# Kernel tuning notes

Measured on AMD Instinct MI355X. Metric: run time of the kernel, lower is better.

## Reference

```python
import jax, jax.numpy as jnp
import numpy as np

WS = 4        # window_size
HEADS = 12    # num_heads


def setup_inputs() -> dict:
    key = jax.random.key(0)
    k1, k2, k3 = jax.random.split(key, 3)
    B, N, E = 32, 4096, 384
    x = jax.random.normal(k1, (B, N, E), dtype=jnp.float32)
    w_in = jax.random.normal(k2, (3 * E, E), dtype=jnp.float32) * 0.02
    b_in = jnp.zeros((3 * E,), dtype=jnp.float32)
    w_out = jax.random.normal(k3, (E, E), dtype=jnp.float32) * 0.02
    b_out = jnp.zeros((E,), dtype=jnp.float32)
    return {"x": x, "w_in": w_in, "b_in": b_in, "w_out": w_out, "b_out": b_out}


def reference(x, w_in, b_in, w_out, b_out):
    B, N, E = x.shape
    H = W = int(np.sqrt(N))
    nh, nw = H // WS, W // WS
    hd = E // HEADS
    T = WS * WS  # tokens per window

    # window partition: [B, H, W, E] -> [B*nh*nw, T, E]
    xw = x.reshape(B, nh, WS, nw, WS, E)
    xw = xw.transpose(0, 1, 3, 2, 4, 5).reshape(-1, T, E)

    # packed QKV projection (torch nn.MultiheadAttention in_proj)
    qkv = xw @ w_in.T + b_in                      # [nWin, T, 3E]
    q, k, v = jnp.split(qkv, 3, axis=-1)          # each [nWin, T, E]

    def split_heads(t):
        return t.reshape(-1, T, HEADS, hd).transpose(0, 2, 1, 3)  # [nWin, h, T, hd]

    q, k, v = split_heads(q), split_heads(k), split_heads(v)
    scale = 1.0 / np.sqrt(hd).astype(np.float32)
    scores = jnp.einsum('whqd,whkd->whqk', q * scale, k)          # [nWin, h, T, T]
    attn = jax.nn.softmax(scores, axis=-1)
    out = jnp.einsum('whqk,whkd->whqd', attn, v)                  # [nWin, h, T, hd]
    out = out.transpose(0, 2, 1, 3).reshape(-1, T, E)
    out = out @ w_out.T + b_out                                   # out_proj

    # window reverse: [B*nh*nw, T, E] -> [B, N, E]
    out = out.reshape(B, nh, nw, WS, WS, E)
    out = out.transpose(0, 1, 3, 2, 4, 5).reshape(B, N, E)
    return out
```

## Files before the change

### kernel.cpp

```cpp
#include <hip/hip_runtime.h>
#include <hip/hip_bf16.h>

typedef __attribute__((ext_vector_type(8))) short short8;
typedef __attribute__((ext_vector_type(4))) float f32x4;

static __device__ __forceinline__ f32x4 MFMA16(short8 a, short8 b, f32x4 c) {
    return __builtin_amdgcn_mfma_f32_16x16x32_bf16(a, b, c, 0, 0, 0);
}
static __device__ __forceinline__ unsigned short f2bf(float f) {
    union { __hip_bfloat16 h; unsigned short u; } c;
    c.h = __float2bfloat16(f);
    return c.u;
}
static __device__ __forceinline__ void gload16(const void* g, void* l) {
    __builtin_amdgcn_global_load_lds(
        (const __attribute__((address_space(1))) unsigned int*)g,
        (__attribute__((address_space(3))) unsigned int*)l, 16, 0, 0);
}

constexpr size_t kWstOff = 0;
constexpr size_t kWosOff = 884736;
constexpr size_t kBrrOff = 1179648;
constexpr size_t kAttOff = 1184256;

__global__ void prep(const float* __restrict__ w_in, const float* __restrict__ b_in,
                     const float* __restrict__ w_out,
                     char* __restrict__ wst, char* __restrict__ wos,
                     float* __restrict__ brr)
{
    const int i = blockIdx.x * 256 + threadIdx.x;
    if (i < 55296) {
        int hp = i / 9216, rem = i % 9216;
        int s = rem / 1536, slot16 = rem % 1536;
        int row = slot16 >> 3, sl = slot16 & 7;
        int c8 = sl ^ (row & 7);
        int hh = row / 96, rr = row % 96;
        int sec = rr >> 5, d = rr & 31;
        int srow = sec * 384 + (hp * 2 + hh) * 32 + d;
        int k0 = s * 64 + c8 * 8;
        const float4* src = (const float4*)(w_in + (size_t)srow * 384 + k0);
        float4 a = src[0], b = src[1];
        uint4 w;
        w.x = f2bf(a.x) | ((unsigned)f2bf(a.y) << 16);
        w.y = f2bf(a.z) | ((unsigned)f2bf(a.w) << 16);
        w.z = f2bf(b.x) | ((unsigned)f2bf(b.y) << 16);
        w.w = f2bf(b.z) | ((unsigned)f2bf(b.w) << 16);
        *(uint4*)(wst + (size_t)i * 16) = w;
    } else {
        int j = i - 55296;
        int nb = j / 6144, rem = j % 6144;
        int s = rem / 1024, slot16 = rem % 1024;
        int row = slot16 >> 3, sl = slot16 & 7;
        int c8 = sl ^ (row & 7);
        int srow = nb * 128 + row;
        int k0 = s * 64 + c8 * 8;
        const float4* src = (const float4*)(w_out + (size_t)srow * 384 + k0);
        float4 a = src[0], b = src[1];
        uint4 w;
        w.x = f2bf(a.x) | ((unsigned)f2bf(a.y) << 16);
        w.y = f2bf(a.z) | ((unsigned)f2bf(a.w) << 16);
        w.z = f2bf(b.x) | ((unsigned)f2bf(b.y) << 16);
        w.w = f2bf(b.z) | ((unsigned)f2bf(b.w) << 16);
        *(uint4*)(wos + (size_t)j * 16) = w;
    }
    if (i < 1152) {
        int h = i / 96, jj = i % 96;
        int sec = jj >> 5, d = jj & 31;
        brr[i] = b_in[sec * 384 + h * 32 + d];
    }
}

__global__ void prep_x(const float* __restrict__ x, char* __restrict__ xbf)
{
    const int i = blockIdx.x * 256 + threadIdx.x;
    const int lane = i & 63;
    const int cc = (i >> 6) & 1;
    const int f = (i >> 7) & 7;
    const int rem = i >> 10;
    const int s = rem % 6, mb = rem / 6;

    int T = mb * 128 + f * 16 + (lane & 15);
    int win = T >> 4, t4 = T & 15;
    int bb = win >> 8, wh = (win >> 4) & 15, ww = win & 15;
    int n = (wh * 4 + (t4 >> 2)) * 64 + ww * 4 + (t4 & 3);
    int k0 = s * 64 + cc * 32 + (lane >> 4) * 8;

    const float4* src = (const float4*)(x + ((size_t)bb * 4096 + n) * 384 + k0);
    float4 a = src[0], b = src[1];
    uint4 w;
    w.x = f2bf(a.x) | ((unsigned)f2bf(a.y) << 16);
    w.y = f2bf(a.z) | ((unsigned)f2bf(a.w) << 16);
    w.z = f2bf(b.x) | ((unsigned)f2bf(b.y) << 16);
    w.w = f2bf(b.z) | ((unsigned)f2bf(b.w) << 16);
    *(uint4*)(xbf + (size_t)i * 16) = w;
}

__global__ __launch_bounds__(512, 2)
void qkv_attn(const char* __restrict__ xbf, const char* __restrict__ wst,
              const float* __restrict__ brr, char* __restrict__ attst)
{
    __shared__ __align__(16) char smem[49152];

    const int tid  = threadIdx.x;
    const int lane = tid & 63, wid = tid >> 6;
    const int g = lane >> 4, r16 = lane & 15;
    const int wm = wid >> 2, wn = wid & 3;

    int b = blockIdx.x;
    int L = (b & 7) * 768 + (b >> 3);
    const int mblk = L / 6, hp = L - mblk * 6;

    const char* xb = xbf + (size_t)mblk * 98304;
    const char* wst_blk = wst + (size_t)hp * 147456;
    auto stage_B = [&](int s, int buf) {
        char* dst = smem + buf * 24576 + tid * 16;
        const char* src = wst_blk + s * 24576 + tid * 16;
        #pragma unroll
        for (int j = 0; j < 3; ++j) gload16(src + j * 8192, dst + j * 8192);
    };

    f32x4 acc[4][3] = {};
    auto compute = [&](int s, int buf) {
        const char* bbp = smem + buf * 24576;
        const char* xs = xb + (size_t)s * 16384 + (size_t)(wm * 8) * 1024 + lane * 16;
        short8 a[4][2];
        #pragma unroll
        for (int mi = 0; mi < 4; ++mi)
            #pragma unroll
            for (int c = 0; c < 2; ++c)
                a[mi][c] = *(const short8*)(xs + (mi * 2 + c) * 1024);
        #pragma unroll
        for (int c = 0; c < 2; ++c) {
            const int sw = ((c * 4 + g) ^ (r16 & 7)) << 4;
            short8 bf[3];
            #pragma unroll
            for (int ni = 0; ni < 3; ++ni)
                bf[ni] = *(const short8*)(bbp + (wn * 48 + ni * 16 + r16) * 128 + sw);
            #pragma unroll
            for (int mi = 0; mi < 4; ++mi)
                #pragma unroll
                for (int ni = 0; ni < 3; ++ni)
                    acc[mi][ni] = MFMA16(a[mi][c], bf[ni], acc[mi][ni]);
        }
    };

    stage_B(0, 0);
    for (int s = 0; s < 6; ++s) {
        __syncthreads();
        if (s < 5) stage_B(s + 1, (s + 1) & 1);
        compute(s, s & 1);
    }
    __syncthreads();

    #pragma unroll
    for (int mi = 0; mi < 4; ++mi) {
        const int win = wm * 4 + mi;
        #pragma unroll
        for (int ni = 0; ni < 3; ++ni) {
            const int cb = wn * 48 + ni * 16;
            const int hl = cb / 96;
            const int w96 = cb - hl * 96;
            const int sec = w96 >> 5;
            const int d = (w96 & 31) + r16;
            const float bias = brr[(hp * 2 + hl) * 96 + w96 + r16];
            float v0 = acc[mi][ni][0] + bias;
            float v1 = acc[mi][ni][1] + bias;
            float v2 = acc[mi][ni][2] + bias;
            float v3 = acc[mi][ni][3] + bias;
            uint2 w;
            w.x = f2bf(v0) | ((unsigned)f2bf(v1) << 16);
            w.y = f2bf(v2) | ((unsigned)f2bf(v3) << 16);
            *(uint2*)(smem + win * 6144 + hl * 3072 + sec * 1024 + d * 32 + g * 8) = w;
        }
    }
    __syncthreads();

    const float kC = 0.17677669529663687f * 1.4426950408889634f;
    const f32x4 zero = {0.f, 0.f, 0.f, 0.f};
    const int win = wid;
    #pragma unroll
    for (int hl = 0; hl < 2; ++hl) {
        char* base = smem + win * 6144 + hl * 3072;

        union U8 { unsigned short e[8]; short8 v; };
        U8 ku, qu;
        #pragma unroll
        for (int j = 0; j < 8; ++j) {
            const int off = (g * 8 + j) * 32 + r16 * 2;
            qu.e[j] = *(const unsigned short*)(base + off);
            ku.e[j] = *(const unsigned short*)(base + 1024 + off);
        }
        f32x4 s = MFMA16(ku.v, qu.v, zero);

        float m = fmaxf(fmaxf(s[0], s[1]), fmaxf(s[2], s[3]));
        m = fmaxf(m, __shfl_xor(m, 16, 64));
        m = fmaxf(m, __shfl_xor(m, 32, 64));
        float p[4], sum = 0.f;
        #pragma unroll
        for (int r = 0; r < 4; ++r) { p[r] = exp2f((s[r] - m) * kC); sum += p[r]; }
        sum += __shfl_xor(sum, 16, 64);
        sum += __shfl_xor(sum, 32, 64);
        const float inv = 1.f / sum;

        U8 pu;
        pu.e[0] = f2bf(p[0] * inv); pu.e[1] = f2bf(p[1] * inv);
        pu.e[2] = f2bf(p[2] * inv); pu.e[3] = f2bf(p[3] * inv);
        pu.e[4] = 0; pu.e[5] = 0; pu.e[6] = 0; pu.e[7] = 0;

        f32x4 o[2];
        #pragma unroll
        for (int ti = 0; ti < 2; ++ti) {
            U8 vu;
            *(uint2*)&vu.e[0] = *(const uint2*)(base + 2048 + (ti * 16 + r16) * 32 + g * 8);
            vu.e[4] = 0; vu.e[5] = 0; vu.e[6] = 0; vu.e[7] = 0;
            o[ti] = MFMA16(pu.v, vu.v, zero);
        }

        #pragma unroll
        for (int ti = 0; ti < 2; ++ti)
            #pragma unroll
            for (int r = 0; r < 4; ++r)
                *(unsigned short*)(base + (g * 4 + r) * 64 + (ti * 16 + r16) * 2)
                    = f2bf(o[ti][r]);
        uint4 ov = *(const uint4*)(base + r16 * 64 + g * 16);

        const int ghead = hp * 2 + hl;
        int row7 = win * 16 + r16;
        int col8 = ghead * 4 + g;
        int sst = col8 >> 3;
        int sl = (col8 & 7) ^ (row7 & 7);
        *(uint4*)(attst + (size_t)mblk * 98304 + sst * 16384 + row7 * 128 + sl * 16) = ov;
    }
}

__global__ __launch_bounds__(256, 2)
void out_proj(const char* __restrict__ attst, const char* __restrict__ wos,
              const float* __restrict__ b_out, float* __restrict__ out)
{
    __shared__ __align__(16) char smem[65536];

    const int tid  = threadIdx.x;
    const int lane = tid & 63, wid = tid >> 6;
    const int g = lane >> 4, r16 = lane & 15;
    const int wm = wid >> 1, wn = wid & 1;

    int b = blockIdx.x;
    int L = (b & 7) * 384 + (b >> 3);
    const int mblk = L / 3, nblk = L - mblk * 3;

    auto stage = [&](int s, int buf) {
        const char* asrc = attst + (size_t)mblk * 98304 + s * 16384 + wid * 4096 + lane * 16;
        const char* bsrc = wos   + (size_t)nblk * 98304 + s * 16384 + wid * 4096 + lane * 16;
        char* adst = smem + buf * 16384 + wid * 4096;
        char* bdst = smem + 32768 + buf * 16384 + wid * 4096;
        #pragma unroll
        for (int j = 0; j < 4; ++j) {
            gload16(asrc + j * 1024, adst + j * 1024);
            gload16(bsrc + j * 1024, bdst + j * 1024);
        }
    };

    f32x4 acc[4][4] = {};
    auto compute = [&](int buf) {
        const char* ab = smem + buf * 16384;
        const char* bbp = smem + 32768 + buf * 16384;
        #pragma unroll
        for (int c = 0; c < 2; ++c) {
            const int sw = ((c * 4 + g) ^ (r16 & 7)) << 4;
            short8 a[4], bf[4];
            #pragma unroll
            for (int mi = 0; mi < 4; ++mi)
                a[mi] = *(const short8*)(ab + (wm * 64 + mi * 16 + r16) * 128 + sw);
            #pragma unroll
            for (int ni = 0; ni < 4; ++ni)
                bf[ni] = *(const short8*)(bbp + (wn * 64 + ni * 16 + r16) * 128 + sw);
            #pragma unroll
            for (int mi = 0; mi < 4; ++mi)
                #pragma unroll
                for (int ni = 0; ni < 4; ++ni)
                    acc[mi][ni] = MFMA16(a[mi], bf[ni], acc[mi][ni]);
        }
    };

    stage(0, 0);
    for (int s = 0; s < 6; ++s) {
        __syncthreads();
        if (s < 5) stage(s + 1, (s + 1) & 1);
        compute(s & 1);
    }

    float bias[4];
    #pragma unroll
    for (int ni = 0; ni < 4; ++ni) bias[ni] = b_out[nblk * 128 + wn * 64 + ni * 16 + r16];

    #pragma unroll
    for (int mi = 0; mi < 4; ++mi) {
        #pragma unroll
        for (int r = 0; r < 4; ++r) {
            int T = mblk * 128 + wm * 64 + mi * 16 + g * 4 + r;
            int win = T >> 4, tt = T & 15;
            int bb = win >> 8, wh = (win >> 4) & 15, ww = win & 15;
            size_t o = ((size_t)bb * 4096 + (wh * 4 + (tt >> 2)) * 64 + ww * 4 + (tt & 3)) * 384
                     + nblk * 128 + wn * 64;
            #pragma unroll
            for (int ni = 0; ni < 4; ++ni)
                out[o + ni * 16 + r16] = acc[mi][ni][r] + bias[ni];
        }
    }
}

extern "C" void kernel_launch(void* const* d_in, const int* in_sizes, int n_in,
                              void* d_out, int out_size, void* d_ws, size_t ws_size,
                              hipStream_t stream) {
    const float* x     = (const float*)d_in[0];
    const float* w_in  = (const float*)d_in[1];
    const float* b_in  = (const float*)d_in[2];
    const float* w_out = (const float*)d_in[3];
    const float* b_out = (const float*)d_in[4];
    float* out = (float*)d_out;

    char* ws = (char*)d_ws;
    char*  wst = ws + kWstOff;
    char*  wos = ws + kWosOff;
    float* brr = (float*)(ws + kBrrOff);
    char*  att = ws + kAttOff;
    char*  xbf = (char*)d_out;

    prep<<<dim3(288), dim3(256), 0, stream>>>(w_in, b_in, w_out, wst, wos, brr);
    prep_x<<<dim3(24576), dim3(256), 0, stream>>>(x, xbf);
    qkv_attn<<<dim3(6144), dim3(512), 0, stream>>>(xbf, wst, brr, att);
    out_proj<<<dim3(3072), dim3(256), 0, stream>>>(att, wos, b_out, out);
}
```

Measured before the change: 309.9 us.

## Remap QKV warp tiling so each warp owns one head, dropping the block barrier

Changes the warp layout in the fused QKV+attention kernel from 2x4 to 4x2. Each warp now computes 2 windows by 96 columns, which is one full head's q/k/v, so the attention phase reads only data the same warp wrote to LDS. That removes a block-wide __syncthreads before attention. It also issues the x A-fragment loads before the next B staging, with a sched_barrier between them, and preloads the bias per head. The cost is a different operand reuse ratio: more B fragments are read per warp and fewer A fragments, with 12 accumulator tiles held either way.

```diff
diff --git a/kernel.cpp b/kernel.cpp
--- a/kernel.cpp
+++ b/kernel.cpp
@@ -104,11 +104,12 @@
     const int tid  = threadIdx.x;
     const int lane = tid & 63, wid = tid >> 6;
     const int g = lane >> 4, r16 = lane & 15;
-    const int wm = wid >> 2, wn = wid & 3;
+    const int wm = wid >> 1, wn = wid & 1;
 
     int b = blockIdx.x;
     int L = (b & 7) * 768 + (b >> 3);
     const int mblk = L / 6, hp = L - mblk * 6;
+    const int head = hp * 2 + wn;
 
     const char* xb = xbf + (size_t)mblk * 98304;
     const char* wst_blk = wst + (size_t)hp * 147456;
@@ -119,68 +120,69 @@
         for (int j = 0; j < 3; ++j) gload16(src + j * 8192, dst + j * 8192);
     };
 
-    f32x4 acc[4][3] = {};
-    auto compute = [&](int s, int buf) {
-        const char* bbp = smem + buf * 24576;
-        const char* xs = xb + (size_t)s * 16384 + (size_t)(wm * 8) * 1024 + lane * 16;
-        short8 a[4][2];
-        #pragma unroll
-        for (int mi = 0; mi < 4; ++mi)
-            #pragma unroll
-            for (int c = 0; c < 2; ++c)
-                a[mi][c] = *(const short8*)(xs + (mi * 2 + c) * 1024);
-        #pragma unroll
-        for (int c = 0; c < 2; ++c) {
-            const int sw = ((c * 4 + g) ^ (r16 & 7)) << 4;
-            short8 bf[3];
-            #pragma unroll
-            for (int ni = 0; ni < 3; ++ni)
-                bf[ni] = *(const short8*)(bbp + (wn * 48 + ni * 16 + r16) * 128 + sw);
-            #pragma unroll
-            for (int mi = 0; mi < 4; ++mi)
-                #pragma unroll
-                for (int ni = 0; ni < 3; ++ni)
-                    acc[mi][ni] = MFMA16(a[mi][c], bf[ni], acc[mi][ni]);
-        }
-    };
+    f32x4 acc[2][6] = {};
 
     stage_B(0, 0);
     for (int s = 0; s < 6; ++s) {
         __syncthreads();
+        short8 a[2][2];
+        {
+            const char* xs = xb + (size_t)s * 16384 + lane * 16;
+            #pragma unroll
+            for (int mi = 0; mi < 2; ++mi)
+                #pragma unroll
+                for (int c = 0; c < 2; ++c)
+                    a[mi][c] = *(const short8*)(xs + ((wm * 2 + mi) * 2048 + c * 1024));
+        }
+        __builtin_amdgcn_sched_barrier(0);
         if (s < 5) stage_B(s + 1, (s + 1) & 1);
-        compute(s, s & 1);
+
+        const char* bbp = smem + (s & 1) * 24576;
+        #pragma unroll
+        for (int c = 0; c < 2; ++c) {
+            const int sw = ((c * 4 + g) ^ (r16 & 7)) << 4;
+            short8 bf[6];
+            #pragma unroll
+            for (int ni = 0; ni < 6; ++ni)
+                bf[ni] = *(const short8*)(bbp + (wn * 96 + ni * 16 + r16) * 128 + sw);
+            #pragma unroll
+            for (int mi = 0; mi < 2; ++mi)
+                #pragma unroll
+                for (int ni = 0; ni < 6; ++ni)
+                    acc[mi][ni] = MFMA16(a[mi][c], bf[ni], acc[mi][ni]);
+        }
     }
     __syncthreads();
 
-    #pragma unroll
-    for (int mi = 0; mi < 4; ++mi) {
-        const int win = wm * 4 + mi;
-        #pragma unroll
-        for (int ni = 0; ni < 3; ++ni) {
-            const int cb = wn * 48 + ni * 16;
-            const int hl = cb / 96;
-            const int w96 = cb - hl * 96;
-            const int sec = w96 >> 5;
-            const int d = (w96 & 31) + r16;
-            const float bias = brr[(hp * 2 + hl) * 96 + w96 + r16];
-            float v0 = acc[mi][ni][0] + bias;
-            float v1 = acc[mi][ni][1] + bias;
-            float v2 = acc[mi][ni][2] + bias;
-            float v3 = acc[mi][ni][3] + bias;
+    float bias[6];
+    #pragma unroll
+    for (int ni = 0; ni < 6; ++ni) bias[ni] = brr[head * 96 + ni * 16 + r16];
+
+    #pragma unroll
+    for (int mi = 0; mi < 2; ++mi) {
+        const int win = wm * 2 + mi;
+        #pragma unroll
+        for (int ni = 0; ni < 6; ++ni) {
+            const int sec = ni >> 1;
+            const int d = (ni & 1) * 16 + r16;
+            float v0 = acc[mi][ni][0] + bias[ni];
+            float v1 = acc[mi][ni][1] + bias[ni];
+            float v2 = acc[mi][ni][2] + bias[ni];
+            float v3 = acc[mi][ni][3] + bias[ni];
             uint2 w;
             w.x = f2bf(v0) | ((unsigned)f2bf(v1) << 16);
             w.y = f2bf(v2) | ((unsigned)f2bf(v3) << 16);
-            *(uint2*)(smem + win * 6144 + hl * 3072 + sec * 1024 + d * 32 + g * 8) = w;
-        }
-    }
-    __syncthreads();
+            *(uint2*)(smem + win * 6144 + wn * 3072 + sec * 1024 + d * 32 + g * 8) = w;
+        }
+    }
 
     const float kC = 0.17677669529663687f * 1.4426950408889634f;
     const f32x4 zero = {0.f, 0.f, 0.f, 0.f};
-    const int win = wid;
-    #pragma unroll
-    for (int hl = 0; hl < 2; ++hl) {
-        char* base = smem + win * 6144 + hl * 3072;
+
+    #pragma unroll
+    for (int i = 0; i < 2; ++i) {
+        const int win = wm * 2 + i;
+        char* base = smem + win * 6144 + wn * 3072;
 
         union U8 { unsigned short e[8]; short8 v; };
         U8 ku, qu;
@@ -224,7 +226,7 @@
                     = f2bf(o[ti][r]);
         uint4 ov = *(const uint4*)(base + r16 * 64 + g * 16);
 
-        const int ghead = hp * 2 + hl;
+        const int ghead = hp * 2 + wn;
         int row7 = win * 16 + r16;
         int col8 = ghead * 4 + g;
         int sst = col8 >> 3;
```

Result: faster. 274.0 us (-11.6%).

## Store Q/K token-major with XOR swizzle and issue A loads before B staging

Applied to the files above, without the earlier changes.

The QKV epilogue now writes Q and K into shared memory token-major with an XOR-swizzled 16-byte slot layout. The attention stage can then fetch each Q/K fragment with one 16-byte LDS load instead of eight 2-byte gathers. The GEMM main loop is inlined, and the global A-fragment loads are issued before the next B stage's async LDS copies, separated by a sched_barrier. The aim is to hide latency and shrink LDS instruction count. In exchange, the epilogue now does four scalar 2-byte stores per Q/K fragment instead of one 8-byte store.

```diff
diff --git a/kernel.cpp b/kernel.cpp
--- a/kernel.cpp
+++ b/kernel.cpp
@@ -120,15 +120,23 @@
     };
 
     f32x4 acc[4][3] = {};
-    auto compute = [&](int s, int buf) {
-        const char* bbp = smem + buf * 24576;
-        const char* xs = xb + (size_t)s * 16384 + (size_t)(wm * 8) * 1024 + lane * 16;
+
+    stage_B(0, 0);
+    for (int s = 0; s < 6; ++s) {
+        __syncthreads();
         short8 a[4][2];
-        #pragma unroll
-        for (int mi = 0; mi < 4; ++mi)
-            #pragma unroll
-            for (int c = 0; c < 2; ++c)
-                a[mi][c] = *(const short8*)(xs + (mi * 2 + c) * 1024);
+        {
+            const char* xs = xb + (size_t)s * 16384 + lane * 16;
+            #pragma unroll
+            for (int mi = 0; mi < 4; ++mi)
+                #pragma unroll
+                for (int c = 0; c < 2; ++c)
+                    a[mi][c] = *(const short8*)(xs + ((wm * 4 + mi) * 2048 + c * 1024));
+        }
+        __builtin_amdgcn_sched_barrier(0);
+        if (s < 5) stage_B(s + 1, (s + 1) & 1);
+
+        const char* bbp = smem + (s & 1) * 24576;
         #pragma unroll
         for (int c = 0; c < 2; ++c) {
             const int sw = ((c * 4 + g) ^ (r16 & 7)) << 4;
@@ -142,13 +150,6 @@
                 for (int ni = 0; ni < 3; ++ni)
                     acc[mi][ni] = MFMA16(a[mi][c], bf[ni], acc[mi][ni]);
         }
-    };
-
-    stage_B(0, 0);
-    for (int s = 0; s < 6; ++s) {
-        __syncthreads();
-        if (s < 5) stage_B(s + 1, (s + 1) & 1);
-        compute(s, s & 1);
     }
     __syncthreads();
 
@@ -163,14 +164,24 @@
             const int sec = w96 >> 5;
             const int d = (w96 & 31) + r16;
             const float bias = brr[(hp * 2 + hl) * 96 + w96 + r16];
+            char* tb = smem + win * 6144 + hl * 3072;
             float v0 = acc[mi][ni][0] + bias;
             float v1 = acc[mi][ni][1] + bias;
             float v2 = acc[mi][ni][2] + bias;
             float v3 = acc[mi][ni][3] + bias;
-            uint2 w;
-            w.x = f2bf(v0) | ((unsigned)f2bf(v1) << 16);
-            w.y = f2bf(v2) | ((unsigned)f2bf(v3) << 16);
-            *(uint2*)(smem + win * 6144 + hl * 3072 + sec * 1024 + d * 32 + g * 8) = w;
+            if (sec < 2) {
+                const int slot16 = d >> 3;
+                const int boff = sec * 1024 + ((slot16 ^ g) * 16) + (d & 7) * 2;
+                *(unsigned short*)(tb + boff + (g * 4 + 0) * 64) = f2bf(v0);
+                *(unsigned short*)(tb + boff + (g * 4 + 1) * 64) = f2bf(v1);
+                *(unsigned short*)(tb + boff + (g * 4 + 2) * 64) = f2bf(v2);
+                *(unsigned short*)(tb + boff + (g * 4 + 3) * 64) = f2bf(v3);
+            } else {
+                uint2 w;
+                w.x = f2bf(v0) | ((unsigned)f2bf(v1) << 16);
+                w.y = f2bf(v2) | ((unsigned)f2bf(v3) << 16);
+                *(uint2*)(tb + 2048 + d * 32 + g * 8) = w;
+            }
         }
     }
     __syncthreads();
@@ -178,19 +189,14 @@
     const float kC = 0.17677669529663687f * 1.4426950408889634f;
     const f32x4 zero = {0.f, 0.f, 0.f, 0.f};
     const int win = wid;
+    const int qsl = (g ^ ((r16 >> 2) & 3)) << 4;
     #pragma unroll
     for (int hl = 0; hl < 2; ++hl) {
         char* base = smem + win * 6144 + hl * 3072;
 
-        union U8 { unsigned short e[8]; short8 v; };
-        U8 ku, qu;
-        #pragma unroll
-        for (int j = 0; j < 8; ++j) {
-            const int off = (g * 8 + j) * 32 + r16 * 2;
-            qu.e[j] = *(const unsigned short*)(base + off);
-            ku.e[j] = *(const unsigned short*)(base + 1024 + off);
-        }
-        f32x4 s = MFMA16(ku.v, qu.v, zero);
+        short8 qv = *(const short8*)(base + r16 * 64 + qsl);
+        short8 kv = *(const short8*)(base + 1024 + r16 * 64 + qsl);
+        f32x4 s = MFMA16(kv, qv, zero);
 
         float m = fmaxf(fmaxf(s[0], s[1]), fmaxf(s[2], s[3]));
         m = fmaxf(m, __shfl_xor(m, 16, 64));
@@ -202,6 +208,7 @@
         sum += __shfl_xor(sum, 32, 64);
         const float inv = 1.f / sum;
 
+        union U8 { unsigned short e[8]; short8 v; };
         U8 pu;
         pu.e[0] = f2bf(p[0] * inv); pu.e[1] = f2bf(p[1] * inv);
         pu.e[2] = f2bf(p[2] * inv); pu.e[3] = f2bf(p[3] * inv);
```

Measured after the change: 280.0 us. 1.11x faster.

## Load QKV weights directly from global in MFMA fragment layout, drop LDS staging

Applied to the files above, without the earlier changes.

The weight prep kernel now writes w_in in the exact per-lane MFMA fragment order. The QKV GEMM then reads B fragments straight from global/L2 instead of staging them through double-buffered LDS with global_load_lds. Each wave now owns one window (16 rows) and computes all 192 columns (12 accumulators), so the later attention stage reads its own LDS tile. This removes the LDS staging traffic and most of the block barriers. In exchange, every wave re-reads the full weight slice from cache and there is no prefetch overlap, and a leftover __syncthreads remains in the loop. Block-to-tile mapping also changes, putting all head pairs of one L2 group together.

```diff
diff --git a/kernel.cpp b/kernel.cpp
--- a/kernel.cpp
+++ b/kernel.cpp
@@ -18,26 +18,28 @@
         (__attribute__((address_space(3))) unsigned int*)l, 16, 0, 0);
 }
 
-constexpr size_t kWstOff = 0;
+constexpr size_t kWbfOff = 0;
 constexpr size_t kWosOff = 884736;
 constexpr size_t kBrrOff = 1179648;
 constexpr size_t kAttOff = 1184256;
 
 __global__ void prep(const float* __restrict__ w_in, const float* __restrict__ b_in,
                      const float* __restrict__ w_out,
-                     char* __restrict__ wst, char* __restrict__ wos,
+                     char* __restrict__ wbf, char* __restrict__ wos,
                      float* __restrict__ brr)
 {
     const int i = blockIdx.x * 256 + threadIdx.x;
     if (i < 55296) {
         int hp = i / 9216, rem = i % 9216;
-        int s = rem / 1536, slot16 = rem % 1536;
-        int row = slot16 >> 3, sl = slot16 & 7;
-        int c8 = sl ^ (row & 7);
+        int s = rem / 1536, t = rem % 1536;
+        int f = t >> 7, rem2 = t & 127;
+        int c = rem2 >> 6, lane = rem2 & 63;
+        int g = lane >> 4, r16 = lane & 15;
+        int row = f * 16 + r16;
         int hh = row / 96, rr = row % 96;
         int sec = rr >> 5, d = rr & 31;
         int srow = sec * 384 + (hp * 2 + hh) * 32 + d;
-        int k0 = s * 64 + c8 * 8;
+        int k0 = s * 64 + c * 32 + g * 8;
         const float4* src = (const float4*)(w_in + (size_t)srow * 384 + k0);
         float4 a = src[0], b = src[1];
         uint4 w;
@@ -45,7 +47,7 @@
         w.y = f2bf(a.z) | ((unsigned)f2bf(a.w) << 16);
         w.z = f2bf(b.x) | ((unsigned)f2bf(b.y) << 16);
         w.w = f2bf(b.z) | ((unsigned)f2bf(b.w) << 16);
-        *(uint4*)(wst + (size_t)i * 16) = w;
+        *(uint4*)(wbf + (size_t)i * 16) = w;
     } else {
         int j = i - 55296;
         int nb = j / 6144, rem = j % 6144;
@@ -96,7 +98,7 @@
 }
 
 __global__ __launch_bounds__(512, 2)
-void qkv_attn(const char* __restrict__ xbf, const char* __restrict__ wst,
+void qkv_attn(const char* __restrict__ xbf, const char* __restrict__ wbf,
               const float* __restrict__ brr, char* __restrict__ attst)
 {
     __shared__ __align__(16) char smem[49152];
@@ -104,91 +106,73 @@
     const int tid  = threadIdx.x;
     const int lane = tid & 63, wid = tid >> 6;
     const int g = lane >> 4, r16 = lane & 15;
-    const int wm = wid >> 2, wn = wid & 3;
 
     int b = blockIdx.x;
-    int L = (b & 7) * 768 + (b >> 3);
-    const int mblk = L / 6, hp = L - mblk * 6;
-
-    const char* xb = xbf + (size_t)mblk * 98304;
-    const char* wst_blk = wst + (size_t)hp * 147456;
-    auto stage_B = [&](int s, int buf) {
-        char* dst = smem + buf * 24576 + tid * 16;
-        const char* src = wst_blk + s * 24576 + tid * 16;
-        #pragma unroll
-        for (int j = 0; j < 3; ++j) gload16(src + j * 8192, dst + j * 8192);
-    };
-
-    f32x4 acc[4][3] = {};
-    auto compute = [&](int s, int buf) {
-        const char* bbp = smem + buf * 24576;
-        const char* xs = xb + (size_t)s * 16384 + (size_t)(wm * 8) * 1024 + lane * 16;
-        short8 a[4][2];
-        #pragma unroll
-        for (int mi = 0; mi < 4; ++mi)
-            #pragma unroll
-            for (int c = 0; c < 2; ++c)
-                a[mi][c] = *(const short8*)(xs + (mi * 2 + c) * 1024);
-        #pragma unroll
-        for (int c = 0; c < 2; ++c) {
-            const int sw = ((c * 4 + g) ^ (r16 & 7)) << 4;
-            short8 bf[3];
-            #pragma unroll
-            for (int ni = 0; ni < 3; ++ni)
-                bf[ni] = *(const short8*)(bbp + (wn * 48 + ni * 16 + r16) * 128 + sw);
-            #pragma unroll
-            for (int mi = 0; mi < 4; ++mi)
-                #pragma unroll
-                for (int ni = 0; ni < 3; ++ni)
-                    acc[mi][ni] = MFMA16(a[mi][c], bf[ni], acc[mi][ni]);
-        }
-    };
-
-    stage_B(0, 0);
+    int x8 = b & 7, j = b >> 3;
+    const int hp = j >> 7;
+    const int mblk = x8 * 128 + (j & 127);
+
+    const char* xw = xbf + (size_t)mblk * 98304 + (size_t)wid * 2048 + lane * 16;
+    const char* bw = wbf + (size_t)hp * 147456 + lane * 16;
+
+    f32x4 acc[12] = {};
+
+    #pragma unroll
     for (int s = 0; s < 6; ++s) {
         __syncthreads();
-        if (s < 5) stage_B(s + 1, (s + 1) & 1);
-        compute(s, s & 1);
-    }
-    __syncthreads();
-
-    #pragma unroll
-    for (int mi = 0; mi < 4; ++mi) {
-        const int win = wm * 4 + mi;
-        #pragma unroll
-        for (int ni = 0; ni < 3; ++ni) {
-            const int cb = wn * 48 + ni * 16;
-            const int hl = cb / 96;
-            const int w96 = cb - hl * 96;
-            const int sec = w96 >> 5;
-            const int d = (w96 & 31) + r16;
-            const float bias = brr[(hp * 2 + hl) * 96 + w96 + r16];
-            float v0 = acc[mi][ni][0] + bias;
-            float v1 = acc[mi][ni][1] + bias;
-            float v2 = acc[mi][ni][2] + bias;
-            float v3 = acc[mi][ni][3] + bias;
-            uint2 w;
-            w.x = f2bf(v0) | ((unsigned)f2bf(v1) << 16);
-            w.y = f2bf(v2) | ((unsigned)f2bf(v3) << 16);
-            *(uint2*)(smem + win * 6144 + hl * 3072 + sec * 1024 + d * 32 + g * 8) = w;
-        }
-    }
-    __syncthreads();
+        short8 a[2];
+        #pragma unroll
+        for (int c = 0; c < 2; ++c)
+            a[c] = *(const short8*)(xw + s * 16384 + c * 1024);
+        #pragma unroll
+        for (int c = 0; c < 2; ++c) {
+            const char* bs = bw + s * 24576 + c * 1024;
+            #pragma unroll
+            for (int nh = 0; nh < 2; ++nh) {
+                short8 bf[6];
+                #pragma unroll
+                for (int k = 0; k < 6; ++k)
+                    bf[k] = *(const short8*)(bs + (nh * 6 + k) * 2048);
+                #pragma unroll
+                for (int k = 0; k < 6; ++k)
+                    acc[nh * 6 + k] = MFMA16(a[c], bf[k], acc[nh * 6 + k]);
+            }
+        }
+    }
+
+    char* tile = smem + wid * 6144;
+    #pragma unroll
+    for (int ni = 0; ni < 12; ++ni) {
+        const int cb = ni * 16;
+        const int hl = cb / 96;
+        const int w96 = cb - hl * 96;
+        const int sec = w96 >> 5;
+        const int d = (w96 & 31) + r16;
+        const float bias = brr[(hp * 2 + hl) * 96 + w96 + r16];
+        float v0 = acc[ni][0] + bias;
+        float v1 = acc[ni][1] + bias;
+        float v2 = acc[ni][2] + bias;
+        float v3 = acc[ni][3] + bias;
+        uint2 w;
+        w.x = f2bf(v0) | ((unsigned)f2bf(v1) << 16);
+        w.y = f2bf(v2) | ((unsigned)f2bf(v3) << 16);
+        *(uint2*)(tile + hl * 3072 + sec * 1024 + d * 32 + g * 8) = w;
+    }
 
     const float kC = 0.17677669529663687f * 1.4426950408889634f;
     const f32x4 zero = {0.f, 0.f, 0.f, 0.f};
     const int win = wid;
     #pragma unroll
     for (int hl = 0; hl < 2; ++hl) {
-        char* base = smem + win * 6144 + hl * 3072;
+        char* base = tile + hl * 3072;
 
         union U8 { unsigned short e[8]; short8 v; };
         U8 ku, qu;
         #pragma unroll
-        for (int j = 0; j < 8; ++j) {
-            const int off = (g * 8 + j) * 32 + r16 * 2;
-            qu.e[j] = *(const unsigned short*)(base + off);
-            ku.e[j] = *(const unsigned short*)(base + 1024 + off);
+        for (int jj = 0; jj < 8; ++jj) {
+            const int off = (g * 8 + jj) * 32 + r16 * 2;
+            qu.e[jj] = *(const unsigned short*)(base + off);
+            ku.e[jj] = *(const unsigned short*)(base + 1024 + off);
         }
         f32x4 s = MFMA16(ku.v, qu.v, zero);
 
@@ -320,14 +304,14 @@
     float* out = (float*)d_out;
 
     char* ws = (char*)d_ws;
-    char*  wst = ws + kWstOff;
+    char*  wbf = ws + kWbfOff;
     char*  wos = ws + kWosOff;
     float* brr = (float*)(ws + kBrrOff);
     char*  att = ws + kAttOff;
     char*  xbf = (char*)d_out;
 
-    prep<<<dim3(288), dim3(256), 0, stream>>>(w_in, b_in, w_out, wst, wos, brr);
+    prep<<<dim3(288), dim3(256), 0, stream>>>(w_in, b_in, w_out, wbf, wos, brr);
     prep_x<<<dim3(24576), dim3(256), 0, stream>>>(x, xbf);
-    qkv_attn<<<dim3(6144), dim3(512), 0, stream>>>(xbf, wst, brr, att);
+    qkv_attn<<<dim3(6144), dim3(512), 0, stream>>>(xbf, wbf, brr, att);
     out_proj<<<dim3(3072), dim3(256), 0, stream>>>(att, wos, b_out, out);
 }
```

Measured after the change: 450.6 us. +45.4%, slower.
